# Kernel optimization log

Hardware: AMD Instinct MI355X
Metric: run time of the kernel (lower is better)

The kernel has to match this reference:

```python
import jax, jax.numpy as jnp
import numpy as np

B, N, K = 4096, 4096, 4  # batch, neurons, num activation fns (=MLP width)

def setup_inputs() -> dict:
    key = jax.random.key(0)
    ks = jax.random.split(key, 5)
    s = jax.random.normal(ks[0], (B, N), dtype=jnp.float32)
    # per-neuron gating MLP params: Linear(K,K) -> sigmoid -> Linear(K,K)
    W1 = jax.random.uniform(ks[1], (N, K, K), minval=-0.5, maxval=0.5, dtype=jnp.float32)
    b1 = jax.random.uniform(ks[2], (N, K), minval=-0.5, maxval=0.5, dtype=jnp.float32)
    W2 = jax.random.uniform(ks[3], (N, K, K), minval=-0.5, maxval=0.5, dtype=jnp.float32)
    b2 = jax.random.uniform(ks[4], (N, K), minval=-0.5, maxval=0.5, dtype=jnp.float32)
    return {"s": s, "W1": W1, "b1": b1, "W2": W2, "b2": b2}

def reference(s, W1, b1, W2, b2):
    # Candidate activations, stacked in ModuleDict iteration order
    # (relu, sigmoid, antirelu, identity) -> [B, N, K]
    acts = jnp.stack([
        jnp.maximum(s, 0.0),      # relu
        jax.nn.sigmoid(s),        # sigmoid
        jnp.minimum(s, 0.0),      # antirelu
        s,                        # identity
    ], axis=-1)
    # Batched per-neuron gating MLP (all N tiny MLPs fused into one einsum)
    h = jax.nn.sigmoid(jnp.einsum('bnk,nkh->bnh', acts, W1) + b1)   # [B, N, K]
    logits = jnp.einsum('bnh,nhk->bnk', h, W2) + b2                 # [B, N, K]
    alpha = jax.nn.softmax(logits, axis=-1)                          # gating weights
    return jnp.sum(alpha * acts, axis=-1)                            # [B, N]
```

## Files before the change

kernel.cpp:

```cpp
#include <hip/hip_runtime.h>


typedef float v2f __attribute__((ext_vector_type(2)));
#define SPL(x) ((v2f)(x))
#define L2E 1.44269504088896340736f
#define TSTRIDE 129

static __device__ __forceinline__ float hexp2(float x){ return __builtin_amdgcn_exp2f(x); }
static __device__ __forceinline__ float hrcp(float x){ return __builtin_amdgcn_rcpf(x); }
static __device__ __forceinline__ float sigm(float z){ return hrcp(1.0f + hexp2(-z*L2E)); }

static __device__ float eval_gate(float x, const float4* w1, const float4 c1,
                                  const float4* w2, const float4 c2) {
    const float a0 = fmaxf(x, 0.f), a2 = fminf(x, 0.f), a3 = x;
    const float a1 = sigm(x);
    const float h0 = sigm(fmaf(a0,w1[0].x, fmaf(a1,w1[1].x, fmaf(a2,w1[2].x, fmaf(a3,w1[3].x, c1.x)))));
    const float h1 = sigm(fmaf(a0,w1[0].y, fmaf(a1,w1[1].y, fmaf(a2,w1[2].y, fmaf(a3,w1[3].y, c1.y)))));
    const float h2 = sigm(fmaf(a0,w1[0].z, fmaf(a1,w1[1].z, fmaf(a2,w1[2].z, fmaf(a3,w1[3].z, c1.z)))));
    const float h3 = sigm(fmaf(a0,w1[0].w, fmaf(a1,w1[1].w, fmaf(a2,w1[2].w, fmaf(a3,w1[3].w, c1.w)))));
    const float l0 = fmaf(h0,w2[0].x, fmaf(h1,w2[1].x, fmaf(h2,w2[2].x, fmaf(h3,w2[3].x, c2.x))));
    const float l1 = fmaf(h0,w2[0].y, fmaf(h1,w2[1].y, fmaf(h2,w2[2].y, fmaf(h3,w2[3].y, c2.y))));
    const float l2 = fmaf(h0,w2[0].z, fmaf(h1,w2[1].z, fmaf(h2,w2[2].z, fmaf(h3,w2[3].z, c2.z))));
    const float l3 = fmaf(h0,w2[0].w, fmaf(h1,w2[1].w, fmaf(h2,w2[2].w, fmaf(h3,w2[3].w, c2.w))));
    const float e0 = hexp2(l0*L2E), e1 = hexp2(l1*L2E), e2 = hexp2(l2*L2E), e3 = hexp2(l3*L2E);
    const float den = (e0+e1)+(e2+e3);
    const float num = fmaf(e0,a0, fmaf(e1,a1, fmaf(e2,a2, e3*a3)));
    return num * hrcp(den);
}

__global__ __launch_bounds__(256) void build_lut(
    const float* __restrict__ W1, const float* __restrict__ b1,
    const float* __restrict__ W2, const float* __restrict__ b2,
    float* __restrict__ tab, int N)
{
    const int gid  = blockIdx.x * 256 + threadIdx.x;
    const int n    = gid >> 6;
    const int lane = gid & 63;
    if (n >= N) return;
    const float4* W1v = (const float4*)W1;
    const float4* W2v = (const float4*)W2;
    float4 w1[4], w2[4];
    #pragma unroll
    for (int k = 0; k < 4; ++k) { w1[k] = W1v[(size_t)n*4 + k]; w2[k] = W2v[(size_t)n*4 + k]; }
    const float4 c1 = ((const float4*)b1)[n];
    const float4 c2 = ((const float4*)b2)[n];

    float* tn = tab + (size_t)n * TSTRIDE;
    const float x0 = fmaf((float)lane, 0.125f, -8.0f);
    const float x1 = fmaf((float)(lane + 64), 0.125f, -8.0f);
    tn[lane]      = eval_gate(x0, w1, c1, w2, c2);
    tn[lane + 64] = eval_gate(x1, w1, c1, w2, c2);
    if (lane == 0) tn[128] = eval_gate(8.0f, w1, c1, w2, c2);
}

__global__ __launch_bounds__(256) void lut_mix(
    const float* __restrict__ s, const float* __restrict__ tab,
    float* __restrict__ out, int B, int N)
{
    __shared__ float lut[64 * TSTRIDE];

    const int lane = threadIdx.x & 63;
    const int warp = threadIdx.x >> 6;
    const int n0   = blockIdx.x * 64;
    const int b0   = blockIdx.y * 128;

    {
        const float* tg = tab + (size_t)n0 * TSTRIDE;
        for (int idx = threadIdx.x; idx < 64 * TSTRIDE; idx += 256)
            lut[idx] = tg[idx];
    }
    __syncthreads();

    const size_t sN = (size_t)N;
    const float* sp = s   + (size_t)(b0 + warp*32) * sN + (n0 + lane);
    float*       op = out + (size_t)(b0 + warp*32) * sN + (n0 + lane);
    const float* tl = lut + lane * TSTRIDE;

    auto load8 = [&](int k, float (&xv)[8]) {
        #pragma unroll
        for (int r = 0; r < 8; ++r)
            xv[r] = sp[(size_t)(k*8 + r) * sN];
    };
    auto compute8 = [&](int k, const float (&xv)[8]) {
        float fr[8], f0[8], f1[8];
        #pragma unroll
        for (int r = 0; r < 8; ++r) {
            const float t  = fmaf(xv[r], 8.0f, 64.0f);
            float i_f = __builtin_amdgcn_fmed3f(floorf(t), 0.0f, 127.0f);
            fr[r] = t - i_f;
            const int i = (int)i_f;
            f0[r] = tl[i];
            f1[r] = tl[i + 1];
        }
        #pragma unroll
        for (int r = 0; r < 8; ++r)
            op[(size_t)(k*8 + r) * sN] = fmaf(fr[r], f1[r] - f0[r], f0[r]);
    };

    float xa[8], xb[8];
    load8(0, xa);
    #pragma unroll 1
    for (int k = 0; k < 4; k += 2) {
        load8(k + 1, xb);
        compute8(k, xa);
        if (k + 2 < 4) load8(k + 2, xa);
        compute8(k + 1, xb);
    }
}

static __device__ __forceinline__ v2f fma2(v2f a, v2f b, v2f c) {
    return __builtin_elementwise_fma(a, b, c);
}
static __device__ __forceinline__ v2f exp2v(v2f y) {
    v2f r; r.x = hexp2(y.x); r.y = hexp2(y.y); return r;
}
static __device__ __forceinline__ v2f rcpv(v2f d) {
    v2f r; r.x = hrcp(d.x); r.y = hrcp(d.y); return r;
}

__global__ __launch_bounds__(256) void gatemix_fb(
    const float* __restrict__ s, const float* __restrict__ W1,
    const float* __restrict__ b1, const float* __restrict__ W2,
    const float* __restrict__ b2, float* __restrict__ out, int B, int N)
{
    const int n = blockIdx.x * 256 + threadIdx.x;
    const float4* W1v = (const float4*)W1;
    const float4* W2v = (const float4*)W2;
    v2f w1[4][4], bb1[4];
    #pragma unroll
    for (int k = 0; k < 4; ++k) {
        float4 rw = W1v[(size_t)n*4 + k];
        w1[k][0] = SPL(rw.x); w1[k][1] = SPL(rw.y);
        w1[k][2] = SPL(rw.z); w1[k][3] = SPL(rw.w);
    }
    { float4 rb = ((const float4*)b1)[n];
      bb1[0]=SPL(rb.x); bb1[1]=SPL(rb.y); bb1[2]=SPL(rb.z); bb1[3]=SPL(rb.w); }
    v2f w2d[4][3], bb2[3];
    #pragma unroll
    for (int j = 0; j < 4; ++j) {
        float4 rw = W2v[(size_t)n*4 + j];
        w2d[j][0] = SPL((rw.x - rw.w) * L2E);
        w2d[j][1] = SPL((rw.y - rw.w) * L2E);
        w2d[j][2] = SPL((rw.z - rw.w) * L2E);
    }
    { float4 rc = ((const float4*)b2)[n];
      bb2[0] = SPL((rc.x - rc.w) * L2E);
      bb2[1] = SPL((rc.y - rc.w) * L2E);
      bb2[2] = SPL((rc.z - rc.w) * L2E); }

    const v2f cn1 = SPL(8.0128205e-3f), cn2 = SPL(4.3706294e-5f), cn3 = SPL(2.8906051e-8f);
    const v2f cd1 = SPL(1.1538462e-1f), cd2 = SPL(1.4568765e-3f), cd3 = SPL(3.2372594e-6f);
    const v2f vQ = SPL(0.25f), vH = SPL(0.5f), vOne = SPL(1.0f);

    const size_t sN = (size_t)N;
    const float* sp = s   + (size_t)(blockIdx.y * 8) * sN + n;
    float*       op = out + (size_t)(blockIdx.y * 8) * sN + n;
    v2f xr[4];
    #pragma unroll
    for (int r = 0; r < 4; ++r) {
        xr[r].x = sp[(size_t)(2*r)   * sN];
        xr[r].y = sp[(size_t)(2*r+1) * sN];
    }
    #pragma unroll
    for (int it = 0; it < 4; ++it) {
        const v2f x = xr[it];
        v2f a0 = __builtin_elementwise_max(x, SPL(0.0f));
        v2f a2 = __builtin_elementwise_min(x, SPL(0.0f));
        v2f u  = x * x;
        v2f pn = fma2(fma2(fma2(cn3, u, cn2), u, cn1), u, vQ);
        v2f pd = fma2(fma2(fma2(cd3, u, cd2), u, cd1), u, vOne);
        v2f a1 = fma2(x * pn, rcpv(pd), vH);
        v2f qd[4], nm[4];
        #pragma unroll
        for (int j = 0; j < 4; ++j) {
            v2f zj = fma2(a0, w1[0][j], fma2(a1, w1[1][j],
                     fma2(a2, w1[2][j], fma2(x,  w1[3][j], bb1[j]))));
            v2f vv = zj * zj;
            v2f nn = fma2(fma2(fma2(cn3, vv, cn2), vv, cn1), vv, vQ);
            qd[j]  = fma2(fma2(fma2(cd3, vv, cd2), vv, cd1), vv, vOne);
            nm[j]  = zj * nn;
        }
        v2f p01 = qd[0] * qd[1], p23 = qd[2] * qd[3];
        v2f rr  = rcpv(p01 * p23);
        v2f i01 = p23 * rr, i23 = p01 * rr;
        v2f h0 = fma2(nm[0] * qd[1], i01, vH);
        v2f h1 = fma2(nm[1] * qd[0], i01, vH);
        v2f h2 = fma2(nm[2] * qd[3], i23, vH);
        v2f h3 = fma2(nm[3] * qd[2], i23, vH);
        v2f l0 = fma2(h0,w2d[0][0], fma2(h1,w2d[1][0], fma2(h2,w2d[2][0], fma2(h3,w2d[3][0], bb2[0]))));
        v2f l1 = fma2(h0,w2d[0][1], fma2(h1,w2d[1][1], fma2(h2,w2d[2][1], fma2(h3,w2d[3][1], bb2[1]))));
        v2f l2 = fma2(h0,w2d[0][2], fma2(h1,w2d[1][2], fma2(h2,w2d[2][2], fma2(h3,w2d[3][2], bb2[2]))));
        v2f e0 = exp2v(l0), e1 = exp2v(l1), e2 = exp2v(l2);
        v2f den = (e0 + e1) + (e2 + vOne);
        v2f num = fma2(e0, a0, fma2(e1, a1, fma2(e2, a2, x)));
        v2f o = num * rcpv(den);
        op[(size_t)(2*it)   * sN] = o.x;
        op[(size_t)(2*it+1) * sN] = o.y;
    }
}

extern "C" void kernel_launch(void* const* d_in, const int* in_sizes, int n_in,
                              void* d_out, int out_size, void* d_ws, size_t ws_size,
                              hipStream_t stream) {
    const float* s  = (const float*)d_in[0];
    const float* W1 = (const float*)d_in[1];
    const float* b1 = (const float*)d_in[2];
    const float* W2 = (const float*)d_in[3];
    const float* b2 = (const float*)d_in[4];
    float* out = (float*)d_out;

    const int K = 4;
    const int N = in_sizes[2] / K;
    const int B = in_sizes[0] / N;

    const size_t tab_bytes = (size_t)N * TSTRIDE * sizeof(float);
    if (ws_size >= tab_bytes && (N % 64) == 0 && (B % 128) == 0) {
        float* tab = (float*)d_ws;
        build_lut<<<dim3((N*64 + 255)/256), 256, 0, stream>>>(W1, b1, W2, b2, tab, N);
        dim3 grid(N / 64, B / 128);
        lut_mix<<<grid, 256, 0, stream>>>(s, tab, out, B, N);
    } else {
        dim3 grid(N / 256, B / 8);
        gatemix_fb<<<grid, 256, 0, stream>>>(s, W1, b1, W2, b2, out, B, N);
    }
}
```

Measured before the change: 31.94 us.

## Vectorize LUT mix to float4 per thread, double rows per block, nontemporal stores

Reworks the LUT-interpolation kernel so each thread handles four adjacent neurons with 128-bit loads and stores instead of scalar accesses. Each block now covers 256 batch rows instead of 128, so the LUT load into shared memory is amortized over twice the work and the grid is halved. Output uses nontemporal stores to avoid polluting cache. LDS lookups now hit four different table rows per thread, which may add bank conflicts, and there are fewer blocks to fill the GPU.

```diff
diff --git a/kernel.cpp b/kernel.cpp
--- a/kernel.cpp
+++ b/kernel.cpp
@@ -2,6 +2,7 @@
 
 
 typedef float v2f __attribute__((ext_vector_type(2)));
+typedef float v4f __attribute__((ext_vector_type(4)));
 #define SPL(x) ((v2f)(x))
 #define L2E 1.44269504088896340736f
 #define TSTRIDE 129
@@ -59,10 +60,10 @@
 {
     __shared__ float lut[64 * TSTRIDE];
 
-    const int lane = threadIdx.x & 63;
-    const int warp = threadIdx.x >> 6;
-    const int n0   = blockIdx.x * 64;
-    const int b0   = blockIdx.y * 128;
+    const int q  = threadIdx.x & 15;
+    const int rb = threadIdx.x >> 4;
+    const int n0 = blockIdx.x * 64;
+    const int b0 = blockIdx.y * 256;
 
     {
         const float* tg = tab + (size_t)n0 * TSTRIDE;
@@ -72,39 +73,47 @@
     __syncthreads();
 
     const size_t sN = (size_t)N;
-    const float* sp = s   + (size_t)(b0 + warp*32) * sN + (n0 + lane);
-    float*       op = out + (size_t)(b0 + warp*32) * sN + (n0 + lane);
-    const float* tl = lut + lane * TSTRIDE;
-
-    auto load8 = [&](int k, float (&xv)[8]) {
+    const float* sp = s   + (size_t)(b0 + rb) * sN + (n0 + 4*q);
+    float*       op = out + (size_t)(b0 + rb) * sN + (n0 + 4*q);
+    const float* tq0 = lut + (4*q + 0) * TSTRIDE;
+    const float* tq1 = lut + (4*q + 1) * TSTRIDE;
+    const float* tq2 = lut + (4*q + 2) * TSTRIDE;
+    const float* tq3 = lut + (4*q + 3) * TSTRIDE;
+
+    auto load4 = [&](int k0, v4f (&xv)[4]) {
         #pragma unroll
-        for (int r = 0; r < 8; ++r)
-            xv[r] = sp[(size_t)(k*8 + r) * sN];
+        for (int k = 0; k < 4; ++k)
+            xv[k] = *(const v4f*)(sp + (size_t)((k0 + k) * 16) * sN);
     };
-    auto compute8 = [&](int k, const float (&xv)[8]) {
-        float fr[8], f0[8], f1[8];
+    auto lerp1 = [&](const float* tl, float x) -> float {
+        const float t   = fmaf(x, 8.0f, 64.0f);
+        const float i_f = __builtin_amdgcn_fmed3f(floorf(t), 0.0f, 127.0f);
+        const float fr  = t - i_f;
+        const int   i   = (int)i_f;
+        const float f0  = tl[i];
+        const float f1  = tl[i + 1];
+        return fmaf(fr, f1 - f0, f0);
+    };
+    auto compute4 = [&](int k0, const v4f (&xv)[4]) {
         #pragma unroll
-        for (int r = 0; r < 8; ++r) {
-            const float t  = fmaf(xv[r], 8.0f, 64.0f);
-            float i_f = __builtin_amdgcn_fmed3f(floorf(t), 0.0f, 127.0f);
-            fr[r] = t - i_f;
-            const int i = (int)i_f;
-            f0[r] = tl[i];
-            f1[r] = tl[i + 1];
+        for (int k = 0; k < 4; ++k) {
+            v4f o;
+            o.x = lerp1(tq0, xv[k].x);
+            o.y = lerp1(tq1, xv[k].y);
+            o.z = lerp1(tq2, xv[k].z);
+            o.w = lerp1(tq3, xv[k].w);
+            __builtin_nontemporal_store(o, (v4f*)(op + (size_t)((k0 + k) * 16) * sN));
         }
-        #pragma unroll
-        for (int r = 0; r < 8; ++r)
-            op[(size_t)(k*8 + r) * sN] = fmaf(fr[r], f1[r] - f0[r], f0[r]);
     };
 
-    float xa[8], xb[8];
-    load8(0, xa);
+    v4f xa[4], xb[4];
+    load4(0, xa);
     #pragma unroll 1
-    for (int k = 0; k < 4; k += 2) {
-        load8(k + 1, xb);
-        compute8(k, xa);
-        if (k + 2 < 4) load8(k + 2, xa);
-        compute8(k + 1, xb);
+    for (int k = 0; k < 16; k += 8) {
+        load4(k + 4, xb);
+        compute4(k, xa);
+        if (k + 8 < 16) load4(k + 8, xa);
+        compute4(k + 4, xb);
     }
 }
 
@@ -214,10 +223,10 @@
     const int B = in_sizes[0] / N;
 
     const size_t tab_bytes = (size_t)N * TSTRIDE * sizeof(float);
-    if (ws_size >= tab_bytes && (N % 64) == 0 && (B % 128) == 0) {
+    if (ws_size >= tab_bytes && (N % 64) == 0 && (B % 256) == 0) {
         float* tab = (float*)d_ws;
         build_lut<<<dim3((N*64 + 255)/256), 256, 0, stream>>>(W1, b1, W2, b2, tab, N);
-        dim3 grid(N / 64, B / 128);
+        dim3 grid(N / 64, B / 256);
         lut_mix<<<grid, 256, 0, stream>>>(s, tab, out, B, N);
     } else {
         dim3 grid(N / 256, B / 8);
```

Measured after the change: 31.99 us. About the same (+0.1%).
